# Optimization experiments

Hardware: AMD Instinct MI355X
Metric: run time of the kernel (lower is better)

## Reference

```python
import jax, jax.numpy as jnp
import numpy as np

KH = KW = 16  # kernel height/width == stride (non-overlapping patches)
E = KH * KW   # Linear in/out features = 256


def setup_inputs() -> dict:
    key = jax.random.key(0)
    k1, k2, k3 = jax.random.split(key, 3)
    H = W = 8192
    data = jax.random.normal(k1, (H, W), dtype=jnp.float32)
    # nn.Linear(E, E): weight (out, in), bias (out,)
    weight = jax.random.normal(k2, (E, E), dtype=jnp.float32) / np.sqrt(E).astype(np.float32)
    bias = jax.random.normal(k3, (E,), dtype=jnp.float32) * 0.01
    return {"data": data, "weight": weight, "bias": bias}


def reference(data, weight, bias):
    # DummyConv forward: for each stride-aligned (16x16) patch,
    # flatten -> Linear(E,E) -> sum -> scalar written to output grid.
    H, W = data.shape
    gh, gw = H // KH, W // KW
    # im2col for non-overlapping patches via reshape/transpose: (gh*gw, E)
    patches = data.reshape(gh, KH, gw, KW).transpose(0, 2, 1, 3).reshape(gh * gw, E)
    # torch Linear: y = x @ W.T + b ; then sum over output features per patch
    y = patches @ weight.T + bias  # (P, E)
    out = jnp.sum(y, axis=-1).reshape(gh, gw)  # (512, 512)
    return out
```

## Files before the change

### kernel.cpp

```cpp
#include <hip/hip_runtime.h>

#define KH 16
#define KW 16
#define E  256

__global__ void DummyConv_prep_kernel(const float* __restrict__ weight,
                                      const float* __restrict__ bias,
                                      float* __restrict__ ws) {
    const int i = threadIdx.x;
    float s = 0.f;
    for (int j = 0; j < E; ++j) s += weight[j * E + i];
    ws[i] = s;
    if (i == 0) {
        float b = 0.f;
        for (int j = 0; j < E; ++j) b += bias[j];
        ws[E] = b;
    }
}

__global__ __launch_bounds__(256) void DummyConv_main_kernel(
    const float* __restrict__ data,
    const float* __restrict__ ws,
    float* __restrict__ out) {
    constexpr int W  = 8192;
    constexpr int GW = 512;

    __shared__ __align__(16) float wsum[E];
    __shared__ float bsum_s;
    __shared__ float partials[64];

    const int t = threadIdx.x;
    wsum[t] = ws[t];
    if (t == 0) bsum_s = ws[E];
    __syncthreads();

    const int tileX = blockIdx.x & 31;
    const int gy    = blockIdx.x >> 5;
    const long rowBase = (long)gy * KH;
    const int  colBase = tileX * 256;

    const int c4    = t & 63;
    const int rquad = t >> 6;
    const int pc    = c4 >> 2;
    const int wcol  = (t & 3) * 4;

    float acc = 0.f;
#pragma unroll
    for (int p = 0; p < 4; ++p) {
        const int r = rquad + p * 4;
        const float4 d = *reinterpret_cast<const float4*>(
            data + (rowBase + r) * (long)W + colBase + c4 * 4);
        const float4 w = *reinterpret_cast<const float4*>(&wsum[r * KW + wcol]);
        acc += d.x * w.x + d.y * w.y + d.z * w.z + d.w * w.w;
    }

    acc += __shfl_xor(acc, 1);
    acc += __shfl_xor(acc, 2);
    if ((t & 3) == 0) partials[pc * 4 + rquad] = acc;
    __syncthreads();

    if (t < 16) {
        const float s = partials[t * 4 + 0] + partials[t * 4 + 1] +
                        partials[t * 4 + 2] + partials[t * 4 + 3] + bsum_s;
        out[(long)gy * GW + tileX * 16 + t] = s;
    }
}

extern "C" void kernel_launch(void* const* d_in, const int* in_sizes, int n_in,
                              void* d_out, int out_size, void* d_ws, size_t ws_size,
                              hipStream_t stream) {
    const float* data   = (const float*)d_in[0];
    const float* weight = (const float*)d_in[1];
    const float* bias   = (const float*)d_in[2];
    float* out = (float*)d_out;
    float* ws  = (float*)d_ws;

    DummyConv_prep_kernel<<<1, 256, 0, stream>>>(weight, bias, ws);

    DummyConv_main_kernel<<<512 * 32, 256, 0, stream>>>(data, ws, out);
}
```

Before: 61.72 us.

## Process four patch rows per block with nontemporal loads and parallelize weight prep

The main kernel now handles four patch rows (64 data rows) per block. This cuts the grid from 16384 to 4096 blocks, loads the summed weights into registers once, and keeps 16 vector loads in flight per thread. Data loads use nontemporal hints because the 256 MB input is streamed once. The prep kernel now uses 1024 threads with coalesced float4 column sums and a shuffle reduction for the bias, replacing a serial single-block loop. The trade-off is fewer blocks to hide latency and higher register use per thread.

```diff
diff --git a/kernel.cpp b/kernel.cpp
--- a/kernel.cpp
+++ b/kernel.cpp
@@ -4,17 +4,39 @@
 #define KW 16
 #define E  256
 
-__global__ void DummyConv_prep_kernel(const float* __restrict__ weight,
-                                      const float* __restrict__ bias,
-                                      float* __restrict__ ws) {
-    const int i = threadIdx.x;
-    float s = 0.f;
-    for (int j = 0; j < E; ++j) s += weight[j * E + i];
-    ws[i] = s;
-    if (i == 0) {
-        float b = 0.f;
-        for (int j = 0; j < E; ++j) b += bias[j];
-        ws[E] = b;
+typedef float f32x4 __attribute__((ext_vector_type(4)));
+
+__global__ __launch_bounds__(1024) void DummyConv_prep_kernel(
+    const float* __restrict__ weight,
+    const float* __restrict__ bias,
+    float* __restrict__ ws) {
+    __shared__ __align__(16) f32x4 red[1024];
+    __shared__ float bred[4];
+
+    const int t  = threadIdx.x;
+    const int c4 = t & 63;
+    const int j0 = t >> 6;
+
+    f32x4 a = {0.f, 0.f, 0.f, 0.f};
+    for (int j = j0; j < E; j += 16) {
+        a += *reinterpret_cast<const f32x4*>(&weight[j * E + c4 * 4]);
+    }
+    red[t] = a;
+
+    if (t < E) {
+        float b = bias[t];
+        b += __shfl_xor(b, 1);  b += __shfl_xor(b, 2);  b += __shfl_xor(b, 4);
+        b += __shfl_xor(b, 8);  b += __shfl_xor(b, 16); b += __shfl_xor(b, 32);
+        if ((t & 63) == 0) bred[t >> 6] = b;
+    }
+    __syncthreads();
+
+    if (t < 64) {
+        f32x4 s = {0.f, 0.f, 0.f, 0.f};
+#pragma unroll
+        for (int k = 0; k < 16; ++k) s += red[k * 64 + t];
+        *reinterpret_cast<f32x4*>(&ws[t * 4]) = s;
+        if (t == 0) ws[E] = bred[0] + bred[1] + bred[2] + bred[3];
     }
 }
 
@@ -27,7 +49,7 @@
 
     __shared__ __align__(16) float wsum[E];
     __shared__ float bsum_s;
-    __shared__ float partials[64];
+    __shared__ float partials[4][64];
 
     const int t = threadIdx.x;
     wsum[t] = ws[t];
@@ -35,8 +57,8 @@
     __syncthreads();
 
     const int tileX = blockIdx.x & 31;
-    const int gy    = blockIdx.x >> 5;
-    const long rowBase = (long)gy * KH;
+    const int gq    = blockIdx.x >> 5;
+    const long rowBase = (long)gq * 64;
     const int  colBase = tileX * 256;
 
     const int c4    = t & 63;
@@ -44,25 +66,38 @@
     const int pc    = c4 >> 2;
     const int wcol  = (t & 3) * 4;
 
-    float acc = 0.f;
+    f32x4 wv[4];
 #pragma unroll
-    for (int p = 0; p < 4; ++p) {
-        const int r = rquad + p * 4;
-        const float4 d = *reinterpret_cast<const float4*>(
-            data + (rowBase + r) * (long)W + colBase + c4 * 4);
-        const float4 w = *reinterpret_cast<const float4*>(&wsum[r * KW + wcol]);
-        acc += d.x * w.x + d.y * w.y + d.z * w.z + d.w * w.w;
+    for (int p = 0; p < 4; ++p)
+        wv[p] = *reinterpret_cast<const f32x4*>(&wsum[(rquad + p * 4) * KW + wcol]);
+
+    float acc[4] = {0.f, 0.f, 0.f, 0.f};
+#pragma unroll
+    for (int pr = 0; pr < 4; ++pr) {
+#pragma unroll
+        for (int p = 0; p < 4; ++p) {
+            const long r = rowBase + pr * 16 + rquad + p * 4;
+            const f32x4 d = __builtin_nontemporal_load(
+                reinterpret_cast<const f32x4*>(data + r * W + colBase + c4 * 4));
+            acc[pr] += d.x * wv[p].x + d.y * wv[p].y + d.z * wv[p].z + d.w * wv[p].w;
+        }
     }
 
-    acc += __shfl_xor(acc, 1);
-    acc += __shfl_xor(acc, 2);
-    if ((t & 3) == 0) partials[pc * 4 + rquad] = acc;
+#pragma unroll
+    for (int pr = 0; pr < 4; ++pr) {
+        float a = acc[pr];
+        a += __shfl_xor(a, 1);
+        a += __shfl_xor(a, 2);
+        if ((t & 3) == 0) partials[pr][pc * 4 + rquad] = a;
+    }
     __syncthreads();
 
-    if (t < 16) {
-        const float s = partials[t * 4 + 0] + partials[t * 4 + 1] +
-                        partials[t * 4 + 2] + partials[t * 4 + 3] + bsum_s;
-        out[(long)gy * GW + tileX * 16 + t] = s;
+    if (t < 64) {
+        const int pr  = t >> 4;
+        const int pcc = t & 15;
+        const float s = partials[pr][pcc * 4 + 0] + partials[pr][pcc * 4 + 1] +
+                        partials[pr][pcc * 4 + 2] + partials[pr][pcc * 4 + 3] + bsum_s;
+        out[((long)gq * 4 + pr) * GW + tileX * 16 + pcc] = s;
     }
 }
 
@@ -75,7 +110,7 @@
     float* out = (float*)d_out;
     float* ws  = (float*)d_ws;
 
-    DummyConv_prep_kernel<<<1, 256, 0, stream>>>(weight, bias, ws);
+    DummyConv_prep_kernel<<<1, 1024, 0, stream>>>(weight, bias, ws);
 
-    DummyConv_main_kernel<<<512 * 32, 256, 0, stream>>>(data, ws, out);
+    DummyConv_main_kernel<<<4096, 256, 0, stream>>>(data, ws, out);
 }
```

Result: faster. 57.20 us (-7.3%).
